# Kernel optimization log

Measured on AMD Instinct MI355X. Metric: run time of the kernel, lower is better.

The kernel has to match this reference:

```python
import jax, jax.numpy as jnp
import numpy as np

N_NODES = 50000
N_EDGES = 800000   # avg degree ~16
IN_CH = 128
HID = 64


def setup_inputs() -> dict:
    key = jax.random.key(0)
    k0, k1, k2, k3 = jax.random.split(key, 4)
    x = jax.random.normal(k0, (N_NODES, IN_CH), dtype=jnp.float32)
    edge_index = jax.random.randint(k1, (2, N_EDGES), 0, N_NODES, dtype=jnp.int32)
    # Glorot-ish init like torch GCNConv
    W1 = jax.random.normal(k2, (IN_CH, HID), dtype=jnp.float32) / np.sqrt(IN_CH).astype(np.float32)
    b1 = jnp.zeros((HID,), dtype=jnp.float32)
    W2 = jax.random.normal(k3, (HID, HID), dtype=jnp.float32) / np.sqrt(HID).astype(np.float32)
    b2 = jnpp = jnp.zeros((HID,), dtype=jnp.float32)
    return {"x": x, "edge_index": edge_index, "W1": W1, "b1": b1, "W2": W2, "b2": b2}


def gcn_conv(x, src, dst, W, b, n):
    """GCNConv with self-loops already appended to (src, dst).
    out = D^{-1/2} (A + I) D^{-1/2} (x @ W) + b, symmetric normalization."""
    h = x @ W                                        # [N, out]
    deg = jax.ops.segment_sum(jnp.ones(src.shape, jnp.float32), dst, num_segments=n)
    dinv = jax.lax.rsqrt(jnp.maximum(deg, 1.0))      # deg >= 1 due to self-loops
    norm = dinv[src] * dinv[dst]                     # [E+N]
    msg = h[src] * norm[:, None]                     # gather + scale
    return jax.ops.segment_sum(msg, dst, num_segments=n) + b


def reference(x, edge_index, W1, b1, W2, b2):
    n = x.shape[0]
    loop = jnp.arange(n, dtype=edge_index.dtype)
    src = jnp.concatenate([edge_index[0], loop])     # add self-loops
    dst = jnp.concatenate([edge_index[1], loop])
    # encode: GCNConv -> ReLU -> GCNConv
    z = jax.nn.relu(gcn_conv(x, src, dst, W1, b1, n))
    z = gcn_conv(z, src, dst, W2, b2, n)
    # decode: gather endpoint embeddings, elementwise product, reduce over hidden
    return (z[edge_index[0]] * z[edge_index[1]]).sum(axis=1)   # [E]
```

## Files before the change

kernel.cpp:

```cpp
#include <hip/hip_runtime.h>
#include <hip/hip_fp16.h>

#define INCH 128
#define HIDC 64
#define CAP  64

typedef int            v4i __attribute__((ext_vector_type(4)));
typedef float          v2f __attribute__((ext_vector_type(2)));
typedef unsigned int   v4u __attribute__((ext_vector_type(4)));

__device__ inline float2 u2f(unsigned int u) {
    return __half22float2(__builtin_bit_cast(__half2, u));
}

__global__ __launch_bounds__(256) void scatter_count_kernel(const int* __restrict__ src,
                                                            const int* __restrict__ dst,
                                                            int* __restrict__ count,
                                                            unsigned short* __restrict__ col,
                                                            int E) {
    int i4 = (blockIdx.x * 256 + threadIdx.x) * 4;
    if (i4 + 3 < E) {
        v4i s = __builtin_nontemporal_load((const v4i*)(src + i4));
        v4i d = __builtin_nontemporal_load((const v4i*)(dst + i4));
        int r0 = atomicAdd(&count[d.x], 1);
        int r1 = atomicAdd(&count[d.y], 1);
        int r2 = atomicAdd(&count[d.z], 1);
        int r3 = atomicAdd(&count[d.w], 1);
        if (r0 < CAP) col[d.x * CAP + r0] = (unsigned short)s.x;
        if (r1 < CAP) col[d.y * CAP + r1] = (unsigned short)s.y;
        if (r2 < CAP) col[d.z * CAP + r2] = (unsigned short)s.z;
        if (r3 < CAP) col[d.w * CAP + r3] = (unsigned short)s.w;
    } else {
        for (int i = i4; i < E; ++i) {
            int d = dst[i];
            int r = atomicAdd(&count[d], 1);
            if (r < CAP) col[d * CAP + r] = (unsigned short)src[i];
        }
    }
}

__global__ __launch_bounds__(128, 2) void gemm1_kernel(const float* __restrict__ x,
                                                       const float* __restrict__ W,
                                                       const int* __restrict__ count,
                                                       __half* __restrict__ hs, int N) {
    int node = (blockIdx.x >> 1) * 128 + threadIdx.x;
    int ch0 = (blockIdx.x & 1) * 32;
    if (node >= N) return;
    const float4* xr = (const float4*)(x + (size_t)node * INCH);
    float acc[32];
    #pragma unroll
    for (int c = 0; c < 32; ++c) acc[c] = 0.f;
    for (int kc = 0; kc < INCH / 4; ++kc) {
        float4 xk = xr[kc];
        const float* wr = W + (kc * 4) * HIDC + ch0;
        #pragma unroll
        for (int ch = 0; ch < 32; ++ch) acc[ch] = fmaf(xk.x, wr[ch], acc[ch]);
        #pragma unroll
        for (int ch = 0; ch < 32; ++ch) acc[ch] = fmaf(xk.y, wr[HIDC + ch], acc[ch]);
        #pragma unroll
        for (int ch = 0; ch < 32; ++ch) acc[ch] = fmaf(xk.z, wr[2 * HIDC + ch], acc[ch]);
        #pragma unroll
        for (int ch = 0; ch < 32; ++ch) acc[ch] = fmaf(xk.w, wr[3 * HIDC + ch], acc[ch]);
    }
    float dn = rsqrtf((float)count[node] + 1.0f);
    v4u hv[4];
    #pragma unroll
    for (int k = 0; k < 4; ++k) {
        #pragma unroll
        for (int e = 0; e < 4; ++e) {
            int c2 = k * 4 + e;
            __half2 h = __float22half2_rn(make_float2(dn * acc[2 * c2], dn * acc[2 * c2 + 1]));
            hv[k][e] = __builtin_bit_cast(unsigned int, h);
        }
    }
    v4u* hr = (v4u*)(hs + (size_t)node * HIDC + ch0);
    #pragma unroll
    for (int k = 0; k < 4; ++k) hr[k] = hv[k];
}

__global__ __launch_bounds__(128, 2) void gemm2_kernel(const float* __restrict__ agg1,
                                                       const float* __restrict__ W,
                                                       const int* __restrict__ count,
                                                       __half* __restrict__ hs, int N) {
    int node = (blockIdx.x >> 1) * 128 + threadIdx.x;
    int ch0 = (blockIdx.x & 1) * 32;
    if (node >= N) return;
    const float4* ar = (const float4*)(agg1 + (size_t)node * HIDC);
    float acc[32];
    #pragma unroll
    for (int c = 0; c < 32; ++c) acc[c] = 0.f;
    for (int kc = 0; kc < HIDC / 4; ++kc) {
        float4 ak = ar[kc];
        float v0 = fmaxf(ak.x, 0.f);
        float v1 = fmaxf(ak.y, 0.f);
        float v2 = fmaxf(ak.z, 0.f);
        float v3 = fmaxf(ak.w, 0.f);
        const float* wr = W + (kc * 4) * HIDC + ch0;
        #pragma unroll
        for (int ch = 0; ch < 32; ++ch) acc[ch] = fmaf(v0, wr[ch], acc[ch]);
        #pragma unroll
        for (int ch = 0; ch < 32; ++ch) acc[ch] = fmaf(v1, wr[HIDC + ch], acc[ch]);
        #pragma unroll
        for (int ch = 0; ch < 32; ++ch) acc[ch] = fmaf(v2, wr[2 * HIDC + ch], acc[ch]);
        #pragma unroll
        for (int ch = 0; ch < 32; ++ch) acc[ch] = fmaf(v3, wr[3 * HIDC + ch], acc[ch]);
    }
    float dn = rsqrtf((float)count[node] + 1.0f);
    v4u hv[4];
    #pragma unroll
    for (int k = 0; k < 4; ++k) {
        #pragma unroll
        for (int e = 0; e < 4; ++e) {
            int c2 = k * 4 + e;
            __half2 h = __float22half2_rn(make_float2(dn * acc[2 * c2], dn * acc[2 * c2 + 1]));
            hv[k][e] = __builtin_bit_cast(unsigned int, h);
        }
    }
    v4u* hr = (v4u*)(hs + (size_t)node * HIDC + ch0);
    #pragma unroll
    for (int k = 0; k < 4; ++k) hr[k] = hv[k];
}

template <int OUT_HALF>
__global__ __launch_bounds__(256) void aggregate_kernel(const int* __restrict__ count,
                                                        const unsigned short* __restrict__ col,
                                                        const __half* __restrict__ hs,
                                                        const float* __restrict__ bias,
                                                        void* __restrict__ agg, int N) {
    int node = blockIdx.x * 8 + (threadIdx.x >> 5);
    int c2 = threadIdx.x & 31;
    if (node >= N) return;
    int cnt = count[node];
    int deg = cnt < CAP ? cnt : CAP;
    const unsigned int* h2p = (const unsigned int*)hs;
    float2 acc = u2f(h2p[(size_t)node * 32 + c2]);
    const unsigned short* row = col + (size_t)node * CAP;
    for (int jb = 0; jb < deg; jb += 16) {
        int s[16];
        unsigned int v[16];
        #pragma unroll
        for (int u = 0; u < 16; ++u) {
            int idx = jb + u;
            s[u] = row[idx < deg ? idx : jb];
        }
        #pragma unroll
        for (int u = 0; u < 16; ++u)
            v[u] = h2p[(size_t)s[u] * 32 + c2];
        #pragma unroll
        for (int u = 0; u < 16; ++u) {
            if (jb + u < deg) {
                float2 f = u2f(v[u]);
                acc.x += f.x; acc.y += f.y;
            }
        }
    }
    float dn = rsqrtf((float)cnt + 1.0f);
    float2 bb = *(const float2*)(bias + c2 * 2);
    float2 r = make_float2(fmaf(acc.x, dn, bb.x), fmaf(acc.y, dn, bb.y));
    if (OUT_HALF) {
        __half2 h = __float22half2_rn(r);
        ((unsigned int*)agg)[(size_t)node * 32 + c2] = __builtin_bit_cast(unsigned int, h);
    } else {
        *(float2*)((float*)agg + (size_t)node * HIDC + c2 * 2) = r;
    }
}

__global__ __launch_bounds__(256) void decode_kernel(const int* __restrict__ src,
                                                     const int* __restrict__ dst,
                                                     const __half* __restrict__ z,
                                                     float* __restrict__ out, int E) {
    long long tid = (long long)blockIdx.x * 256 + threadIdx.x;
    int g = (int)(tid >> 3);
    int q = threadIdx.x & 7;
    int e0 = g * 2;
    if (e0 >= E) return;
    bool has1 = (e0 + 1 < E);
    int s0, d0, s1, d1;
    if (has1) {
        int2 sv = *(const int2*)(src + e0);
        int2 dv = *(const int2*)(dst + e0);
        s0 = sv.x; s1 = sv.y; d0 = dv.x; d1 = dv.y;
    } else {
        s0 = src[e0]; d0 = dst[e0]; s1 = s0; d1 = d0;
    }
    const v4u* z8 = (const v4u*)z;
    v4u a0 = z8[(size_t)s0 * 8 + q];
    v4u b0 = z8[(size_t)d0 * 8 + q];
    v4u a1 = z8[(size_t)s1 * 8 + q];
    v4u b1 = z8[(size_t)d1 * 8 + q];
    float p0 = 0.f, p1 = 0.f;
    #pragma unroll
    for (int k = 0; k < 4; ++k) {
        float2 fa0 = u2f(a0[k]);
        float2 fb0 = u2f(b0[k]);
        float2 fa1 = u2f(a1[k]);
        float2 fb1 = u2f(b1[k]);
        p0 = fmaf(fa0.x, fb0.x, p0); p0 = fmaf(fa0.y, fb0.y, p0);
        p1 = fmaf(fa1.x, fb1.x, p1); p1 = fmaf(fa1.y, fb1.y, p1);
    }
    #pragma unroll
    for (int m = 4; m; m >>= 1) {
        p0 += __shfl_xor(p0, m, 64);
        p1 += __shfl_xor(p1, m, 64);
    }
    if (q == 0) {
        if (has1) {
            v2f r; r.x = p0; r.y = p1;
            __builtin_nontemporal_store(r, (v2f*)(out + e0));
        } else {
            out[e0] = p0;
        }
    }
}

extern "C" void kernel_launch(void* const* d_in, const int* in_sizes, int n_in,
                              void* d_out, int out_size, void* d_ws, size_t ws_size,
                              hipStream_t stream) {
    const float* x  = (const float*)d_in[0];
    const int*   ei = (const int*)d_in[1];
    const float* W1 = (const float*)d_in[2];
    const float* b1 = (const float*)d_in[3];
    const float* W2 = (const float*)d_in[4];
    const float* b2 = (const float*)d_in[5];
    float* out = (float*)d_out;

    const int hid  = in_sizes[3];
    const int inch = in_sizes[2] / hid;
    const int N    = in_sizes[0] / inch;
    const int E    = in_sizes[1] / 2;
    const int* srcp = ei;
    const int* dstp = ei + E;

    char* p = (char*)d_ws;
    auto alloc = [&](size_t bytes) { char* r = p; p += (bytes + 255) & ~(size_t)255; return r; };
    int*            count = (int*)alloc((size_t)N * 4);
    unsigned short* col   = (unsigned short*)alloc((size_t)N * CAP * 2);
    __half*         h1s   = (__half*)alloc((size_t)N * HIDC * 2);
    __half*         h2s   = (__half*)alloc((size_t)N * HIDC * 2);
    __half*         zt    = (__half*)alloc((size_t)N * HIDC * 2);
    float*          agg1  = (float*)alloc((size_t)N * HIDC * 4);

    (void)hipMemsetAsync(count, 0, (size_t)N * 4, stream);

    int edgeBlocks = (E / 4 + 255) / 256 + 1;
    scatter_count_kernel<<<edgeBlocks, 256, 0, stream>>>(srcp, dstp, count, col, E);

    int gemmGrid = 2 * ((N + 127) / 128);
    gemm1_kernel<<<gemmGrid, 128, 0, stream>>>(x, W1, count, h1s, N);
    aggregate_kernel<0><<<(N + 7) / 8, 256, 0, stream>>>(count, col, h1s, b1, agg1, N);
    gemm2_kernel<<<gemmGrid, 128, 0, stream>>>(agg1, W2, count, h2s, N);
    aggregate_kernel<1><<<(N + 7) / 8, 256, 0, stream>>>(count, col, h2s, b2, zt, N);

    long long groups = ((long long)E + 1) / 2;
    long long blocksD = (groups * 8 + 255) / 256;
    decode_kernel<<<(int)blocksD, 256, 0, stream>>>(srcp, dstp, zt, out, E);
}
```

Before: 219.2 us.

## Fuse edge scatter with first GEMM and store layer-1 aggregate in half

The edge scatter/count and the first dense GEMM now share one launch, with the block index choosing the role, so the compute-bound GEMM can overlap the atomic-heavy scatter. Because the degree normalisation is not yet known during the GEMM, a separate scale kernel afterwards rescales h1 in place. The layer-1 aggregate is also stored in fp16 instead of fp32, halving its write and the second GEMM's read. The cost is an extra launch plus a read-modify-write pass over h1, an extra fp16 rounding before scaling, and lower precision for the intermediate.

```diff
diff --git a/kernel.cpp b/kernel.cpp
--- a/kernel.cpp
+++ b/kernel.cpp
@@ -12,55 +12,115 @@
 __device__ inline float2 u2f(unsigned int u) {
     return __half22float2(__builtin_bit_cast(__half2, u));
 }
-
-__global__ __launch_bounds__(256) void scatter_count_kernel(const int* __restrict__ src,
-                                                            const int* __restrict__ dst,
-                                                            int* __restrict__ count,
-                                                            unsigned short* __restrict__ col,
-                                                            int E) {
-    int i4 = (blockIdx.x * 256 + threadIdx.x) * 4;
-    if (i4 + 3 < E) {
-        v4i s = __builtin_nontemporal_load((const v4i*)(src + i4));
-        v4i d = __builtin_nontemporal_load((const v4i*)(dst + i4));
-        int r0 = atomicAdd(&count[d.x], 1);
-        int r1 = atomicAdd(&count[d.y], 1);
-        int r2 = atomicAdd(&count[d.z], 1);
-        int r3 = atomicAdd(&count[d.w], 1);
-        if (r0 < CAP) col[d.x * CAP + r0] = (unsigned short)s.x;
-        if (r1 < CAP) col[d.y * CAP + r1] = (unsigned short)s.y;
-        if (r2 < CAP) col[d.z * CAP + r2] = (unsigned short)s.z;
-        if (r3 < CAP) col[d.w * CAP + r3] = (unsigned short)s.w;
+__device__ inline unsigned int f2u(float a, float b) {
+    __half2 h = __float22half2_rn(make_float2(a, b));
+    return __builtin_bit_cast(unsigned int, h);
+}
+
+__global__ __launch_bounds__(256, 2) void build_gemm1_kernel(const int* __restrict__ src,
+                                                             const int* __restrict__ dst,
+                                                             int* __restrict__ count,
+                                                             unsigned short* __restrict__ col,
+                                                             const float* __restrict__ x,
+                                                             const float* __restrict__ W,
+                                                             __half* __restrict__ hs,
+                                                             int E, int N, int EB) {
+    if ((int)blockIdx.x < EB) {
+        int i4 = ((int)blockIdx.x * 256 + threadIdx.x) * 4;
+        if (i4 + 3 < E) {
+            v4i s = __builtin_nontemporal_load((const v4i*)(src + i4));
+            v4i d = __builtin_nontemporal_load((const v4i*)(dst + i4));
+            int r0 = atomicAdd(&count[d.x], 1);
+            int r1 = atomicAdd(&count[d.y], 1);
+            int r2 = atomicAdd(&count[d.z], 1);
+            int r3 = atomicAdd(&count[d.w], 1);
+            if (r0 < CAP) col[d.x * CAP + r0] = (unsigned short)s.x;
+            if (r1 < CAP) col[d.y * CAP + r1] = (unsigned short)s.y;
+            if (r2 < CAP) col[d.z * CAP + r2] = (unsigned short)s.z;
+            if (r3 < CAP) col[d.w * CAP + r3] = (unsigned short)s.w;
+        } else {
+            for (int i = i4; i < E; ++i) {
+                int d = dst[i];
+                int r = atomicAdd(&count[d], 1);
+                if (r < CAP) col[d * CAP + r] = (unsigned short)src[i];
+            }
+        }
     } else {
-        for (int i = i4; i < E; ++i) {
-            int d = dst[i];
-            int r = atomicAdd(&count[d], 1);
-            if (r < CAP) col[d * CAP + r] = (unsigned short)src[i];
-        }
-    }
-}
-
-__global__ __launch_bounds__(128, 2) void gemm1_kernel(const float* __restrict__ x,
+        int nb = (int)blockIdx.x - EB;
+        int node = nb * 128 + (threadIdx.x & 127);
+        int ch0 = (threadIdx.x >> 7) * 32;
+        if (node >= N) return;
+        const float4* xr = (const float4*)(x + (size_t)node * INCH);
+        float acc[32];
+        #pragma unroll
+        for (int c = 0; c < 32; ++c) acc[c] = 0.f;
+        for (int kc = 0; kc < INCH / 4; ++kc) {
+            float4 xk = xr[kc];
+            const float* wr = W + (kc * 4) * HIDC + ch0;
+            #pragma unroll
+            for (int ch = 0; ch < 32; ++ch) acc[ch] = fmaf(xk.x, wr[ch], acc[ch]);
+            #pragma unroll
+            for (int ch = 0; ch < 32; ++ch) acc[ch] = fmaf(xk.y, wr[HIDC + ch], acc[ch]);
+            #pragma unroll
+            for (int ch = 0; ch < 32; ++ch) acc[ch] = fmaf(xk.z, wr[2 * HIDC + ch], acc[ch]);
+            #pragma unroll
+            for (int ch = 0; ch < 32; ++ch) acc[ch] = fmaf(xk.w, wr[3 * HIDC + ch], acc[ch]);
+        }
+        v4u hv[4];
+        #pragma unroll
+        for (int k = 0; k < 4; ++k) {
+            #pragma unroll
+            for (int e = 0; e < 4; ++e) {
+                int c2 = k * 4 + e;
+                hv[k][e] = f2u(acc[2 * c2], acc[2 * c2 + 1]);
+            }
+        }
+        v4u* hr = (v4u*)(hs + (size_t)node * HIDC + ch0);
+        #pragma unroll
+        for (int k = 0; k < 4; ++k) hr[k] = hv[k];
+    }
+}
+
+__global__ __launch_bounds__(256) void scale_kernel(const int* __restrict__ count,
+                                                    __half* __restrict__ hs, int N) {
+    int idx = (int)blockIdx.x * 256 + threadIdx.x;
+    if (idx >= N * 8) return;
+    int node = idx >> 3;
+    float dn = rsqrtf((float)count[node] + 1.0f);
+    v4u v = ((const v4u*)hs)[idx];
+    v4u o;
+    #pragma unroll
+    for (int k = 0; k < 4; ++k) {
+        float2 f = u2f(v[k]);
+        o[k] = f2u(dn * f.x, dn * f.y);
+    }
+    ((v4u*)hs)[idx] = o;
+}
+
+__global__ __launch_bounds__(128, 2) void gemm2_kernel(const __half* __restrict__ agg1,
                                                        const float* __restrict__ W,
                                                        const int* __restrict__ count,
                                                        __half* __restrict__ hs, int N) {
     int node = (blockIdx.x >> 1) * 128 + threadIdx.x;
     int ch0 = (blockIdx.x & 1) * 32;
     if (node >= N) return;
-    const float4* xr = (const float4*)(x + (size_t)node * INCH);
+    const v4u* ar = (const v4u*)(agg1 + (size_t)node * HIDC);
     float acc[32];
     #pragma unroll
     for (int c = 0; c < 32; ++c) acc[c] = 0.f;
-    for (int kc = 0; kc < INCH / 4; ++kc) {
-        float4 xk = xr[kc];
-        const float* wr = W + (kc * 4) * HIDC + ch0;
-        #pragma unroll
-        for (int ch = 0; ch < 32; ++ch) acc[ch] = fmaf(xk.x, wr[ch], acc[ch]);
-        #pragma unroll
-        for (int ch = 0; ch < 32; ++ch) acc[ch] = fmaf(xk.y, wr[HIDC + ch], acc[ch]);
-        #pragma unroll
-        for (int ch = 0; ch < 32; ++ch) acc[ch] = fmaf(xk.z, wr[2 * HIDC + ch], acc[ch]);
-        #pragma unroll
-        for (int ch = 0; ch < 32; ++ch) acc[ch] = fmaf(xk.w, wr[3 * HIDC + ch], acc[ch]);
+    for (int kc = 0; kc < HIDC / 8; ++kc) {
+        v4u av = ar[kc];
+        #pragma unroll
+        for (int k2 = 0; k2 < 4; ++k2) {
+            float2 f = u2f(av[k2]);
+            float v0 = fmaxf(f.x, 0.f);
+            float v1 = fmaxf(f.y, 0.f);
+            const float* wr = W + (kc * 8 + k2 * 2) * HIDC + ch0;
+            #pragma unroll
+            for (int ch = 0; ch < 32; ++ch) acc[ch] = fmaf(v0, wr[ch], acc[ch]);
+            #pragma unroll
+            for (int ch = 0; ch < 32; ++ch) acc[ch] = fmaf(v1, wr[HIDC + ch], acc[ch]);
+        }
     }
     float dn = rsqrtf((float)count[node] + 1.0f);
     v4u hv[4];
@@ -69,8 +129,7 @@
         #pragma unroll
         for (int e = 0; e < 4; ++e) {
             int c2 = k * 4 + e;
-            __half2 h = __float22half2_rn(make_float2(dn * acc[2 * c2], dn * acc[2 * c2 + 1]));
-            hv[k][e] = __builtin_bit_cast(unsigned int, h);
+            hv[k][e] = f2u(dn * acc[2 * c2], dn * acc[2 * c2 + 1]);
         }
     }
     v4u* hr = (v4u*)(hs + (size_t)node * HIDC + ch0);
@@ -78,55 +137,11 @@
     for (int k = 0; k < 4; ++k) hr[k] = hv[k];
 }
 
-__global__ __launch_bounds__(128, 2) void gemm2_kernel(const float* __restrict__ agg1,
-                                                       const float* __restrict__ W,
-                                                       const int* __restrict__ count,
-                                                       __half* __restrict__ hs, int N) {
-    int node = (blockIdx.x >> 1) * 128 + threadIdx.x;
-    int ch0 = (blockIdx.x & 1) * 32;
-    if (node >= N) return;
-    const float4* ar = (const float4*)(agg1 + (size_t)node * HIDC);
-    float acc[32];
-    #pragma unroll
-    for (int c = 0; c < 32; ++c) acc[c] = 0.f;
-    for (int kc = 0; kc < HIDC / 4; ++kc) {
-        float4 ak = ar[kc];
-        float v0 = fmaxf(ak.x, 0.f);
-        float v1 = fmaxf(ak.y, 0.f);
-        float v2 = fmaxf(ak.z, 0.f);
-        float v3 = fmaxf(ak.w, 0.f);
-        const float* wr = W + (kc * 4) * HIDC + ch0;
-        #pragma unroll
-        for (int ch = 0; ch < 32; ++ch) acc[ch] = fmaf(v0, wr[ch], acc[ch]);
-        #pragma unroll
-        for (int ch = 0; ch < 32; ++ch) acc[ch] = fmaf(v1, wr[HIDC + ch], acc[ch]);
-        #pragma unroll
-        for (int ch = 0; ch < 32; ++ch) acc[ch] = fmaf(v2, wr[2 * HIDC + ch], acc[ch]);
-        #pragma unroll
-        for (int ch = 0; ch < 32; ++ch) acc[ch] = fmaf(v3, wr[3 * HIDC + ch], acc[ch]);
-    }
-    float dn = rsqrtf((float)count[node] + 1.0f);
-    v4u hv[4];
-    #pragma unroll
-    for (int k = 0; k < 4; ++k) {
-        #pragma unroll
-        for (int e = 0; e < 4; ++e) {
-            int c2 = k * 4 + e;
-            __half2 h = __float22half2_rn(make_float2(dn * acc[2 * c2], dn * acc[2 * c2 + 1]));
-            hv[k][e] = __builtin_bit_cast(unsigned int, h);
-        }
-    }
-    v4u* hr = (v4u*)(hs + (size_t)node * HIDC + ch0);
-    #pragma unroll
-    for (int k = 0; k < 4; ++k) hr[k] = hv[k];
-}
-
-template <int OUT_HALF>
 __global__ __launch_bounds__(256) void aggregate_kernel(const int* __restrict__ count,
                                                         const unsigned short* __restrict__ col,
                                                         const __half* __restrict__ hs,
                                                         const float* __restrict__ bias,
-                                                        void* __restrict__ agg, int N) {
+                                                        __half* __restrict__ agg, int N) {
     int node = blockIdx.x * 8 + (threadIdx.x >> 5);
     int c2 = threadIdx.x & 31;
     if (node >= N) return;
@@ -156,13 +171,8 @@
     }
     float dn = rsqrtf((float)cnt + 1.0f);
     float2 bb = *(const float2*)(bias + c2 * 2);
-    float2 r = make_float2(fmaf(acc.x, dn, bb.x), fmaf(acc.y, dn, bb.y));
-    if (OUT_HALF) {
-        __half2 h = __float22half2_rn(r);
-        ((unsigned int*)agg)[(size_t)node * 32 + c2] = __builtin_bit_cast(unsigned int, h);
-    } else {
-        *(float2*)((float*)agg + (size_t)node * HIDC + c2 * 2) = r;
-    }
+    ((unsigned int*)agg)[(size_t)node * 32 + c2] =
+        f2u(fmaf(acc.x, dn, bb.x), fmaf(acc.y, dn, bb.y));
 }
 
 __global__ __launch_bounds__(256) void decode_kernel(const int* __restrict__ src,
@@ -238,18 +248,20 @@
     __half*         h1s   = (__half*)alloc((size_t)N * HIDC * 2);
     __half*         h2s   = (__half*)alloc((size_t)N * HIDC * 2);
     __half*         zt    = (__half*)alloc((size_t)N * HIDC * 2);
-    float*          agg1  = (float*)alloc((size_t)N * HIDC * 4);
+    __half*         agg1  = (__half*)alloc((size_t)N * HIDC * 2);
 
     (void)hipMemsetAsync(count, 0, (size_t)N * 4, stream);
 
-    int edgeBlocks = (E / 4 + 255) / 256 + 1;
-    scatter_count_kernel<<<edgeBlocks, 256, 0, stream>>>(srcp, dstp, count, col, E);
-
+    int EB = (E / 4 + 255) / 256 + 1;
+    int GB = (N + 127) / 128;
+    build_gemm1_kernel<<<EB + GB, 256, 0, stream>>>(srcp, dstp, count, col,
+                                                    x, W1, h1s, E, N, EB);
+    scale_kernel<<<(N * 8 + 255) / 256, 256, 0, stream>>>(count, h1s, N);
+
+    aggregate_kernel<<<(N + 7) / 8, 256, 0, stream>>>(count, col, h1s, b1, agg1, N);
     int gemmGrid = 2 * ((N + 127) / 128);
-    gemm1_kernel<<<gemmGrid, 128, 0, stream>>>(x, W1, count, h1s, N);
-    aggregate_kernel<0><<<(N + 7) / 8, 256, 0, stream>>>(count, col, h1s, b1, agg1, N);
     gemm2_kernel<<<gemmGrid, 128, 0, stream>>>(agg1, W2, count, h2s, N);
-    aggregate_kernel<1><<<(N + 7) / 8, 256, 0, stream>>>(count, col, h2s, b2, zt, N);
+    aggregate_kernel<<<(N + 7) / 8, 256, 0, stream>>>(count, col, h2s, b2, zt, N);
 
     long long groups = ((long long)E + 1) / 2;
     long long blocksD = (groups * 8 + 255) / 256;
```

After: 273.0 us. +24.5%, slower.
